# Kernel tuning notes

Measured on AMD Instinct MI355X. Metric: run time of the kernel, lower is better.

Reference implementation:

```python
import jax, jax.numpy as jnp
import numpy as np

NUM_HEADS = 8
EPS = 1e-5


def setup_inputs() -> dict:
    key = jax.random.key(0)
    ks = jax.random.split(key, 7)
    B, C, H, W, D = 1, 256, 16, 16, 16
    return {
        "x": jax.random.normal(ks[0], (B, C, H, W, D), dtype=jnp.float32),
        "w_dw": jax.random.normal(ks[1], (C, 1, 3, 3, 3), dtype=jnp.float32) * 0.05,
        "b_dw": jax.random.normal(ks[2], (C,), dtype=jnp.float32) * 0.05,
        "w_qkv": jax.random.normal(ks[3], (3 * C, C), dtype=jnp.float32) * 0.05,
        "b_qkv": jax.random.normal(ks[4], (3 * C,), dtype=jnp.float32) * 0.05,
        "w_proj": jax.random.normal(ks[5], (C, C), dtype=jnp.float32) * 0.05,
        "b_proj": jax.random.normal(ks[6], (C,), dtype=jnp.float32) * 0.05,
    }


def reference(x, w_dw, b_dw, w_qkv, b_qkv, w_proj, b_proj):
    B, C, H, W, D = x.shape
    nh = NUM_HEADS
    hd = C // nh
    scale = hd ** (-0.5)
    N = H * W * D

    # depthwise 3x3x3 conv (groups=C), SAME padding
    y = jax.lax.conv_general_dilated(
        x, w_dw, window_strides=(1, 1, 1), padding="SAME",
        dimension_numbers=("NCHWD", "OIHWD", "NCHWD"),
        feature_group_count=C,
    ) + b_dw[None, :, None, None, None]

    # InstanceNorm3d (affine=False): normalize over spatial dims per (b, c)
    mu = y.mean(axis=(2, 3, 4), keepdims=True)
    var = y.var(axis=(2, 3, 4), keepdims=True)
    y = (y - mu) * jax.lax.rsqrt(var + EPS)

    # 1x1x1 conv -> 3*C channels
    qkv = jnp.einsum("bchwd,oc->bohwd", y, w_qkv) + b_qkv[None, :, None, None, None]

    # [B, 3, nh, hd, N] -> q, k, v each [B, nh, N, hd]
    qkv = qkv.reshape(B, 3, nh, hd, N)
    q, k, v = jnp.transpose(qkv, (1, 0, 2, 4, 3))

    attn = jax.nn.softmax(jnp.einsum("bhnd,bhmd->bhnm", q, k) * scale, axis=-1)
    out = jnp.einsum("bhnm,bhmd->bhnd", attn, v)  # [B, nh, N, hd]

    # transpose(-1, -2) then reshape to [B, C, H, W, D]
    out = jnp.transpose(out, (0, 1, 3, 2)).reshape(B, C, H, W, D)

    # output 1x1x1 projection
    out = jnp.einsum("bchwd,oc->bohwd", out, w_proj) + b_proj[None, :, None, None, None]
    return out
```

## Files before the change

kernel.cpp:

```cpp
#include <hip/hip_runtime.h>
#include <hip/hip_bf16.h>

#define NSP 4096
#define QSC2 0.25503486f

typedef __attribute__((ext_vector_type(8))) short bf16x8;
typedef __attribute__((ext_vector_type(4))) float f32x4;
typedef __attribute__((ext_vector_type(16))) float f32x16;

__device__ __forceinline__ unsigned short f2bf(float f){
  union{float f;unsigned int u;}c; c.f=f;
  unsigned int r = c.u + 0x7fffu + ((c.u>>16)&1u);
  return (unsigned short)(r>>16);
}
__device__ __forceinline__ unsigned int pk2(float a, float b){
  __hip_bfloat162 p = __float22bfloat162_rn(make_float2(a, b));
  unsigned int r; __builtin_memcpy(&r, &p, 4); return r;
}
__device__ __forceinline__ ushort4 pk4(float a, float b, float c, float d){
  union { ushort4 u4; uint2 u2; } u;
  u.u2.x = pk2(a, b); u.u2.y = pk2(c, d);
  return u.u4;
}
__device__ __forceinline__ float bfu2f(unsigned short u){
  union { unsigned int i; float f; } c; c.i = ((unsigned int)u) << 16; return c.f;
}

__global__ __launch_bounds__(512) void k_dwconv(
    const float* __restrict__ x,
    const float* __restrict__ wdw,
    unsigned short* __restrict__ ybn)
{
  const int c = blockIdx.x;
  const int tid = threadIdx.x;
  __shared__ float xs[4096];
  __shared__ float wsh[27];
  __shared__ float rs[8], rq[8];

  const float* xc = x + (size_t)c * NSP;
  {
    const float4 a = ((const float4*)xc)[tid*2];
    const float4 b = ((const float4*)xc)[tid*2 + 1];
    *(float4*)&xs[tid*8]     = a;
    *(float4*)&xs[tid*8 + 4] = b;
  }
  if (tid < 27) wsh[tid] = wdw[c*27 + tid];
  __syncthreads();

  const int h = tid >> 5, w = (tid >> 1) & 15, d0 = (tid & 1) * 8;
  float acc[8] = {};
  #pragma unroll
  for (int kh = 0; kh < 3; kh++){
    const int hh = h + kh - 1;
    if ((unsigned)hh >= 16u) continue;
    #pragma unroll
    for (int kw = 0; kw < 3; kw++){
      const int ww = w + kw - 1;
      if ((unsigned)ww >= 16u) continue;
      const float* rowp = &xs[((hh << 4) + ww) << 4];
      float win[10];
      const float4 c0 = *(const float4*)&rowp[d0];
      const float4 c1 = *(const float4*)&rowp[d0 + 4];
      win[1] = c0.x; win[2] = c0.y; win[3] = c0.z; win[4] = c0.w;
      win[5] = c1.x; win[6] = c1.y; win[7] = c1.z; win[8] = c1.w;
      const float e7 = rowp[7], e8 = rowp[8];
      win[0] = d0 ? e7 : 0.f;
      win[9] = d0 ? 0.f : e8;
      #pragma unroll
      for (int kd = 0; kd < 3; kd++){
        const float wv = wsh[kh*9 + kw*3 + kd];
        #pragma unroll
        for (int j = 0; j < 8; j++) acc[j] += wv * win[j + kd];
      }
    }
  }

  float sum = 0.f, sumsq = 0.f;
  #pragma unroll
  for (int j = 0; j < 8; j++){ sum += acc[j]; sumsq += acc[j]*acc[j]; }
  #pragma unroll
  for (int off = 32; off > 0; off >>= 1){
    sum   += __shfl_down(sum, off, 64);
    sumsq += __shfl_down(sumsq, off, 64);
  }
  const int wid = tid >> 6, lane = tid & 63;
  if (lane == 0){ rs[wid] = sum; rq[wid] = sumsq; }
  __syncthreads();
  float ts = 0.f, tq = 0.f;
  #pragma unroll
  for (int i = 0; i < 8; i++){ ts += rs[i]; tq += rq[i]; }
  const float mean = ts * (1.f/4096.f);
  const float var  = tq * (1.f/4096.f) - mean*mean;
  const float rinv = rsqrtf(var + 1e-5f);

  unsigned short* yo = ybn + (size_t)c * NSP + tid*8;
  *(ushort4*)yo =
      pk4((acc[0]-mean)*rinv, (acc[1]-mean)*rinv, (acc[2]-mean)*rinv, (acc[3]-mean)*rinv);
  *(ushort4*)(yo + 4) =
      pk4((acc[4]-mean)*rinv, (acc[5]-mean)*rinv, (acc[6]-mean)*rinv, (acc[7]-mean)*rinv);
}

__global__ __launch_bounds__(256) void k_trans(
    const unsigned short* __restrict__ ybn,
    unsigned short* __restrict__ ynT)
{
  __shared__ unsigned short T[64][72];
  const int tid = threadIdx.x;
  const int n0 = blockIdx.x * 64, c0 = blockIdx.y * 64;
  const int cl = tid >> 4, n4 = (tid & 15) * 4;
  #pragma unroll
  for (int i = 0; i < 4; i++){
    const int c = cl + i*16;
    const ushort4 v = *(const ushort4*)(ybn + (size_t)(c0 + c) * NSP + n0 + n4);
    T[n4+0][c] = v.x; T[n4+1][c] = v.y; T[n4+2][c] = v.z; T[n4+3][c] = v.w;
  }
  __syncthreads();
  const int nl = tid >> 2, s8 = (tid & 3) * 16;
  *(uint4*)(ynT + (size_t)(n0+nl)*256 + c0 + s8)     = *(const uint4*)&T[nl][s8];
  *(uint4*)(ynT + (size_t)(n0+nl)*256 + c0 + s8 + 8) = *(const uint4*)&T[nl][s8 + 8];
}

__global__ __launch_bounds__(256) void k_qkv(
    const float* __restrict__ wqkv,
    const float* __restrict__ bqkv,
    const unsigned short* __restrict__ ynT,
    unsigned short* __restrict__ qb, unsigned short* __restrict__ kb,
    unsigned short* __restrict__ vbt)
{
  __shared__ unsigned short Wb[64][264];
  __shared__ float bsh[64];
  const int tid = threadIdx.x;
  const int o0 = blockIdx.y * 64;
  const int n0 = blockIdx.x * 64;
  {
    const int row = tid & 63, part = tid >> 6;
    const float* src = wqkv + (size_t)(o0 + row) * 256 + part * 64;
    unsigned short* dst = &Wb[row][part*64];
    #pragma unroll
    for (int j = 0; j < 8; j++){
      const float4 a = ((const float4*)src)[2*j];
      const float4 b = ((const float4*)src)[2*j+1];
      *(ushort4*)&dst[j*8]     = pk4(a.x, a.y, a.z, a.w);
      *(ushort4*)&dst[j*8 + 4] = pk4(b.x, b.y, b.z, b.w);
    }
    if (tid < 64) bsh[tid] = bqkv[o0 + tid];
  }
  __syncthreads();

  const int w = tid >> 6, lane = tid & 63, quad = lane >> 4, cc = lane & 15;
  const int nbase = n0 + w*16;
  const bool isv = (o0 >= 512);
  f32x4 acc[4] = {};

  #pragma unroll
  for (int k = 0; k < 8; k++){
    const bf16x8 y0 = *(const bf16x8*)(ynT + (size_t)(nbase + cc) * 256 + k*32 + quad*8);
    #pragma unroll
    for (int os = 0; os < 4; os++){
      const bf16x8 wf = *(const bf16x8*)&Wb[os*16 + cc][k*32 + quad*8];
      if (!isv) acc[os] = __builtin_amdgcn_mfma_f32_16x16x32_bf16(wf, y0, acc[os], 0, 0, 0);
      else      acc[os] = __builtin_amdgcn_mfma_f32_16x16x32_bf16(y0, wf, acc[os], 0, 0, 0);
    }
  }

  if (!isv){
    #pragma unroll
    for (int os = 0; os < 4; os++){
      const int obase = o0 + os*16 + quad*4;
      const int g = obase >> 8, hh = (obase >> 5) & 7, dd0 = obase & 31;
      const int n = nbase + cc;
      unsigned short* dst = (g == 0) ? qb : kb;
      const float sc = (g == 0) ? QSC2 : 1.f;
      const int bb = os*16 + quad*4;
      *(ushort4*)&dst[((size_t)hh * NSP + n) * 32 + dd0] =
          pk4((acc[os][0] + bsh[bb+0]) * sc, (acc[os][1] + bsh[bb+1]) * sc,
              (acc[os][2] + bsh[bb+2]) * sc, (acc[os][3] + bsh[bb+3]) * sc);
    }
  } else {
    #pragma unroll
    for (int os = 0; os < 4; os++){
      const int orow = o0 - 512 + os*16 + cc;
      const float bias = bsh[os*16 + cc];
      const int n4 = nbase + quad*4;
      *(ushort4*)&vbt[(size_t)orow * NSP + n4] =
          pk4(acc[os][0] + bias, acc[os][1] + bias, acc[os][2] + bias, acc[os][3] + bias);
    }
  }
}

__global__ __launch_bounds__(256) void k_attn(
    const unsigned short* __restrict__ qb,
    const unsigned short* __restrict__ kb,
    const unsigned short* __restrict__ vbt,
    unsigned short* __restrict__ opb, float* __restrict__ lp, int ktlen)
{
  const int h = blockIdx.y, q0 = blockIdx.x * 128, z = blockIdx.z;
  const int tid = threadIdx.x;
  const int w = tid >> 6, l = tid & 63;
  const int lq = l & 31, lb = l >> 5;

  __shared__ unsigned short ks [64][40];
  __shared__ unsigned short vsT[32][72];
  __shared__ unsigned short pst[128][72];

  const int qg = q0 + w*32 + lq;
  const bf16x8 qf0 = *(const bf16x8*)(qb + ((size_t)(h*NSP + qg))*32 + lb*8);
  const bf16x8 qf1 = *(const bf16x8*)(qb + ((size_t)(h*NSP + qg))*32 + 16 + lb*8);
  const unsigned short* kbase = kb  + (size_t)h * NSP * 32;
  const unsigned short* vbase = vbt + (size_t)h * 32 * NSP;

  f32x16 oacc = {};
  float lsum = 0.f;

  const int kt0 = z * ktlen;
  const int krow = tid >> 2, kseg = (tid & 3) * 8;
  const int vrow = tid >> 3, vseg = (tid & 7) * 8;
  const int iters = ktlen >> 6;

  for (int it = 0; it < iters; it++){
    const int kt = kt0 + it * 64;
    {
      *(uint4*)&ks[krow][kseg]  = *(const uint4*)(kbase + (size_t)(kt + krow) * 32 + kseg);
      *(uint4*)&vsT[vrow][vseg] = *(const uint4*)(vbase + (size_t)vrow * NSP + kt + vseg);
    }
    __syncthreads();

    #pragma unroll
    for (int t2 = 0; t2 < 2; t2++){
      const bf16x8 af0 = *(const bf16x8*)&ks[t2*32 + lq][lb*8];
      const bf16x8 af1 = *(const bf16x8*)&ks[t2*32 + lq][16 + lb*8];
      f32x16 sa = {};
      sa = __builtin_amdgcn_mfma_f32_32x32x16_bf16(af0, qf0, sa, 0, 0, 0);
      sa = __builtin_amdgcn_mfma_f32_32x32x16_bf16(af1, qf1, sa, 0, 0, 0);
      #pragma unroll
      for (int g = 0; g < 4; g++){
        const float p0 = __builtin_amdgcn_exp2f(sa[g*4+0]);
        const float p1 = __builtin_amdgcn_exp2f(sa[g*4+1]);
        const float p2 = __builtin_amdgcn_exp2f(sa[g*4+2]);
        const float p3 = __builtin_amdgcn_exp2f(sa[g*4+3]);
        lsum += (p0 + p1) + (p2 + p3);
        *(ushort4*)&pst[w*32 + lq][t2*32 + g*8 + lb*4] = pk4(p0, p1, p2, p3);
      }
    }
    #pragma unroll
    for (int ck = 0; ck < 4; ck++){
      const bf16x8 vf = *(const bf16x8*)&vsT[lq]       [ck*16 + lb*8];
      const bf16x8 pf = *(const bf16x8*)&pst[w*32 + lq][ck*16 + lb*8];
      oacc = __builtin_amdgcn_mfma_f32_32x32x16_bf16(vf, pf, oacc, 0, 0, 0);
    }
    __syncthreads();
  }

  lsum += __shfl_xor(lsum, 32, 64);

  unsigned short* dst = opb + ((size_t)z * NSP + qg) * 256 + h*32;
  #pragma unroll
  for (int g = 0; g < 4; g++){
    *(ushort4*)(dst + g*8 + lb*4) =
        pk4(oacc[g*4+0], oacc[g*4+1], oacc[g*4+2], oacc[g*4+3]);
  }
  if (lb == 0) lp[((size_t)z * 8 + h) * NSP + qg] = lsum;
}

__global__ __launch_bounds__(256) void k_proj(
    const float* __restrict__ wproj,
    const float* __restrict__ bproj,
    const unsigned short* __restrict__ opb,
    const float* __restrict__ lp,
    float* __restrict__ out, int nz)
{
  __shared__ unsigned short Wb[64][264];
  const int tid = threadIdx.x;
  const int o0 = blockIdx.y * 64;
  const int n0 = blockIdx.x * 64;
  {
    const int row = tid & 63, part = tid >> 6;
    const float* src = wproj + (size_t)(o0 + row) * 256 + part * 64;
    unsigned short* dst = &Wb[row][part*64];
    #pragma unroll
    for (int j = 0; j < 8; j++){
      const float4 a = ((const float4*)src)[2*j];
      const float4 b = ((const float4*)src)[2*j+1];
      *(ushort4*)&dst[j*8]     = pk4(a.x, a.y, a.z, a.w);
      *(ushort4*)&dst[j*8 + 4] = pk4(b.x, b.y, b.z, b.w);
    }
  }
  __syncthreads();

  const int w = tid >> 6, lane = tid & 63, quad = lane >> 4, cc = lane & 15;
  const int nbase = n0 + w*16;
  const int nr = nbase + cc;
  f32x4 acc[4] = {};

  #pragma unroll
  for (int k = 0; k < 8; k++){
    float lt = 0.f;
    float s[8] = {};
    for (int z = 0; z < nz; z++){
      lt += lp[((size_t)z*8 + k) * NSP + nr];
      union { uint4 q; unsigned short u[8]; } v;
      v.q = *(const uint4*)(opb + ((size_t)z * NSP + nr) * 256 + k*32 + quad*8);
      #pragma unroll
      for (int j = 0; j < 8; j++) s[j] += bfu2f(v.u[j]);
    }
    const float r = 1.f / lt;
    union { bf16x8 v; ushort4 u[2]; } yb;
    yb.u[0] = pk4(s[0]*r, s[1]*r, s[2]*r, s[3]*r);
    yb.u[1] = pk4(s[4]*r, s[5]*r, s[6]*r, s[7]*r);
    #pragma unroll
    for (int os = 0; os < 4; os++){
      const bf16x8 wf = *(const bf16x8*)&Wb[os*16 + cc][k*32 + quad*8];
      acc[os] = __builtin_amdgcn_mfma_f32_16x16x32_bf16(yb.v, wf, acc[os], 0, 0, 0);
    }
  }

  #pragma unroll
  for (int os = 0; os < 4; os++){
    const int o = o0 + os*16 + cc;
    const float bias = bproj[o];
    const int n4 = nbase + quad*4;
    *(float4*)&out[(size_t)o * NSP + n4] =
        make_float4(acc[os][0] + bias, acc[os][1] + bias,
                    acc[os][2] + bias, acc[os][3] + bias);
  }
}

extern "C" void kernel_launch(void* const* d_in, const int* in_sizes, int n_in,
                              void* d_out, int out_size, void* d_ws, size_t ws_size,
                              hipStream_t stream) {
  (void)in_sizes; (void)n_in; (void)out_size;
  const float* x     = (const float*)d_in[0];
  const float* wdw   = (const float*)d_in[1];
  const float* bdw   = (const float*)d_in[2];  (void)bdw;
  const float* wqkv  = (const float*)d_in[3];
  const float* bqkv  = (const float*)d_in[4];
  const float* wproj = (const float*)d_in[5];
  const float* bproj = (const float*)d_in[6];
  float* out = (float*)d_out;

  const int nz = (ws_size >= ((size_t)16 << 20)) ? 4 : 2;
  const int ktlen = NSP / nz;

  char* ws = (char*)d_ws;
  const size_t opB = (size_t)nz << 21;
  unsigned short* opb = (unsigned short*)ws;
  unsigned short* ybn = (unsigned short*)ws;
  unsigned short* ynT = (unsigned short*)(ws + (2<<20));
  unsigned short* qb  = (unsigned short*)(ws + opB);
  unsigned short* kb  = (unsigned short*)(ws + opB + (2<<20));
  unsigned short* vbt = (unsigned short*)(ws + opB + (4<<20));
  float*          lp  = (float*)(ws + opB + (6<<20));

  k_dwconv <<<dim3(256),        dim3(512), 0, stream>>>(x, wdw, ybn);
  k_trans  <<<dim3(64, 4),      dim3(256), 0, stream>>>(ybn, ynT);
  k_qkv    <<<dim3(64, 12),     dim3(256), 0, stream>>>(wqkv, bqkv, ynT, qb, kb, vbt);
  k_attn   <<<dim3(32, 8, nz),  dim3(256), 0, stream>>>(qb, kb, vbt, opb, lp, ktlen);
  k_proj   <<<dim3(64, 4),      dim3(256), 0, stream>>>(wproj, bproj, opb, lp, out, nz);
}
```

Baseline: 145.5 us.

## Fuse transpose into QKV kernel, widen dwconv blocks, split proj output tiles

Removes the separate transpose kernel. The QKV GEMM now loads its 64-token by 256-channel activation tile from the channel-major buffer and transposes it in shared memory, which saves one launch and a 2 MB round trip through global memory. The depthwise conv now runs 1024 threads per channel, each computing 4 outputs, and the projection kernel uses 32-row output tiles to double its grid. The costs are extra shared memory and redundant transposed loads in the QKV kernel (each tile is reloaded by 12 output blocks), strided 8-byte global reads, and bank conflicts on the scalar shared stores.

```diff
diff --git a/kernel.cpp b/kernel.cpp
--- a/kernel.cpp
+++ b/kernel.cpp
@@ -26,7 +26,7 @@
   union { unsigned int i; float f; } c; c.i = ((unsigned int)u) << 16; return c.f;
 }
 
-__global__ __launch_bounds__(512) void k_dwconv(
+__global__ __launch_bounds__(1024) void k_dwconv(
     const float* __restrict__ x,
     const float* __restrict__ wdw,
     unsigned short* __restrict__ ybn)
@@ -35,20 +35,15 @@
   const int tid = threadIdx.x;
   __shared__ float xs[4096];
   __shared__ float wsh[27];
-  __shared__ float rs[8], rq[8];
+  __shared__ float rs[16], rq[16];
 
   const float* xc = x + (size_t)c * NSP;
-  {
-    const float4 a = ((const float4*)xc)[tid*2];
-    const float4 b = ((const float4*)xc)[tid*2 + 1];
-    *(float4*)&xs[tid*8]     = a;
-    *(float4*)&xs[tid*8 + 4] = b;
-  }
+  *(float4*)&xs[tid*4] = ((const float4*)xc)[tid];
   if (tid < 27) wsh[tid] = wdw[c*27 + tid];
   __syncthreads();
 
-  const int h = tid >> 5, w = (tid >> 1) & 15, d0 = (tid & 1) * 8;
-  float acc[8] = {};
+  const int h = tid >> 6, w = (tid >> 2) & 15, d0 = (tid & 3) * 4;
+  float acc[4] = {};
   #pragma unroll
   for (int kh = 0; kh < 3; kh++){
     const int hh = h + kh - 1;
@@ -58,26 +53,23 @@
       const int ww = w + kw - 1;
       if ((unsigned)ww >= 16u) continue;
       const float* rowp = &xs[((hh << 4) + ww) << 4];
-      float win[10];
+      float win[6];
       const float4 c0 = *(const float4*)&rowp[d0];
-      const float4 c1 = *(const float4*)&rowp[d0 + 4];
       win[1] = c0.x; win[2] = c0.y; win[3] = c0.z; win[4] = c0.w;
-      win[5] = c1.x; win[6] = c1.y; win[7] = c1.z; win[8] = c1.w;
-      const float e7 = rowp[7], e8 = rowp[8];
-      win[0] = d0 ? e7 : 0.f;
-      win[9] = d0 ? 0.f : e8;
+      win[0] = d0        ? rowp[d0 - 1] : 0.f;
+      win[5] = (d0 < 12) ? rowp[d0 + 4] : 0.f;
       #pragma unroll
       for (int kd = 0; kd < 3; kd++){
         const float wv = wsh[kh*9 + kw*3 + kd];
         #pragma unroll
-        for (int j = 0; j < 8; j++) acc[j] += wv * win[j + kd];
+        for (int j = 0; j < 4; j++) acc[j] += wv * win[j + kd];
       }
     }
   }
 
   float sum = 0.f, sumsq = 0.f;
   #pragma unroll
-  for (int j = 0; j < 8; j++){ sum += acc[j]; sumsq += acc[j]*acc[j]; }
+  for (int j = 0; j < 4; j++){ sum += acc[j]; sumsq += acc[j]*acc[j]; }
   #pragma unroll
   for (int off = 32; off > 0; off >>= 1){
     sum   += __shfl_down(sum, off, 64);
@@ -88,46 +80,24 @@
   __syncthreads();
   float ts = 0.f, tq = 0.f;
   #pragma unroll
-  for (int i = 0; i < 8; i++){ ts += rs[i]; tq += rq[i]; }
+  for (int i = 0; i < 16; i++){ ts += rs[i]; tq += rq[i]; }
   const float mean = ts * (1.f/4096.f);
   const float var  = tq * (1.f/4096.f) - mean*mean;
   const float rinv = rsqrtf(var + 1e-5f);
 
-  unsigned short* yo = ybn + (size_t)c * NSP + tid*8;
-  *(ushort4*)yo =
+  *(ushort4*)(ybn + (size_t)c * NSP + tid*4) =
       pk4((acc[0]-mean)*rinv, (acc[1]-mean)*rinv, (acc[2]-mean)*rinv, (acc[3]-mean)*rinv);
-  *(ushort4*)(yo + 4) =
-      pk4((acc[4]-mean)*rinv, (acc[5]-mean)*rinv, (acc[6]-mean)*rinv, (acc[7]-mean)*rinv);
-}
-
-__global__ __launch_bounds__(256) void k_trans(
-    const unsigned short* __restrict__ ybn,
-    unsigned short* __restrict__ ynT)
-{
-  __shared__ unsigned short T[64][72];
-  const int tid = threadIdx.x;
-  const int n0 = blockIdx.x * 64, c0 = blockIdx.y * 64;
-  const int cl = tid >> 4, n4 = (tid & 15) * 4;
-  #pragma unroll
-  for (int i = 0; i < 4; i++){
-    const int c = cl + i*16;
-    const ushort4 v = *(const ushort4*)(ybn + (size_t)(c0 + c) * NSP + n0 + n4);
-    T[n4+0][c] = v.x; T[n4+1][c] = v.y; T[n4+2][c] = v.z; T[n4+3][c] = v.w;
-  }
-  __syncthreads();
-  const int nl = tid >> 2, s8 = (tid & 3) * 16;
-  *(uint4*)(ynT + (size_t)(n0+nl)*256 + c0 + s8)     = *(const uint4*)&T[nl][s8];
-  *(uint4*)(ynT + (size_t)(n0+nl)*256 + c0 + s8 + 8) = *(const uint4*)&T[nl][s8 + 8];
 }
 
 __global__ __launch_bounds__(256) void k_qkv(
     const float* __restrict__ wqkv,
     const float* __restrict__ bqkv,
-    const unsigned short* __restrict__ ynT,
+    const unsigned short* __restrict__ ybn,
     unsigned short* __restrict__ qb, unsigned short* __restrict__ kb,
     unsigned short* __restrict__ vbt)
 {
   __shared__ unsigned short Wb[64][264];
+  __shared__ unsigned short Ys[64][264];
   __shared__ float bsh[64];
   const int tid = threadIdx.x;
   const int o0 = blockIdx.y * 64;
@@ -145,6 +115,15 @@
     }
     if (tid < 64) bsh[tid] = bqkv[o0 + tid];
   }
+  {
+    const int cl = tid >> 4, n4 = (tid & 15) * 4;
+    #pragma unroll
+    for (int i = 0; i < 16; i++){
+      const int c = cl * 16 + i;
+      const ushort4 v = *(const ushort4*)(ybn + (size_t)c * NSP + n0 + n4);
+      Ys[n4+0][c] = v.x; Ys[n4+1][c] = v.y; Ys[n4+2][c] = v.z; Ys[n4+3][c] = v.w;
+    }
+  }
   __syncthreads();
 
   const int w = tid >> 6, lane = tid & 63, quad = lane >> 4, cc = lane & 15;
@@ -154,7 +133,7 @@
 
   #pragma unroll
   for (int k = 0; k < 8; k++){
-    const bf16x8 y0 = *(const bf16x8*)(ynT + (size_t)(nbase + cc) * 256 + k*32 + quad*8);
+    const bf16x8 y0 = *(const bf16x8*)&Ys[w*16 + cc][k*32 + quad*8];
     #pragma unroll
     for (int os = 0; os < 4; os++){
       const bf16x8 wf = *(const bf16x8*)&Wb[os*16 + cc][k*32 + quad*8];
@@ -269,16 +248,16 @@
     const float* __restrict__ lp,
     float* __restrict__ out, int nz)
 {
-  __shared__ unsigned short Wb[64][264];
+  __shared__ unsigned short Wb[32][264];
   const int tid = threadIdx.x;
-  const int o0 = blockIdx.y * 64;
+  const int o0 = blockIdx.y * 32;
   const int n0 = blockIdx.x * 64;
   {
-    const int row = tid & 63, part = tid >> 6;
-    const float* src = wproj + (size_t)(o0 + row) * 256 + part * 64;
-    unsigned short* dst = &Wb[row][part*64];
-    #pragma unroll
-    for (int j = 0; j < 8; j++){
+    const int row = tid & 31, part = tid >> 5;
+    const float* src = wproj + (size_t)(o0 + row) * 256 + part * 32;
+    unsigned short* dst = &Wb[row][part*32];
+    #pragma unroll
+    for (int j = 0; j < 4; j++){
       const float4 a = ((const float4*)src)[2*j];
       const float4 b = ((const float4*)src)[2*j+1];
       *(ushort4*)&dst[j*8]     = pk4(a.x, a.y, a.z, a.w);
@@ -290,7 +269,7 @@
   const int w = tid >> 6, lane = tid & 63, quad = lane >> 4, cc = lane & 15;
   const int nbase = n0 + w*16;
   const int nr = nbase + cc;
-  f32x4 acc[4] = {};
+  f32x4 acc[2] = {};
 
   #pragma unroll
   for (int k = 0; k < 8; k++){
@@ -308,14 +287,14 @@
     yb.u[0] = pk4(s[0]*r, s[1]*r, s[2]*r, s[3]*r);
     yb.u[1] = pk4(s[4]*r, s[5]*r, s[6]*r, s[7]*r);
     #pragma unroll
-    for (int os = 0; os < 4; os++){
+    for (int os = 0; os < 2; os++){
       const bf16x8 wf = *(const bf16x8*)&Wb[os*16 + cc][k*32 + quad*8];
       acc[os] = __builtin_amdgcn_mfma_f32_16x16x32_bf16(yb.v, wf, acc[os], 0, 0, 0);
     }
   }
 
   #pragma unroll
-  for (int os = 0; os < 4; os++){
+  for (int os = 0; os < 2; os++){
     const int o = o0 + os*16 + cc;
     const float bias = bproj[o];
     const int n4 = nbase + quad*4;
@@ -345,15 +324,13 @@
   const size_t opB = (size_t)nz << 21;
   unsigned short* opb = (unsigned short*)ws;
   unsigned short* ybn = (unsigned short*)ws;
-  unsigned short* ynT = (unsigned short*)(ws + (2<<20));
   unsigned short* qb  = (unsigned short*)(ws + opB);
   unsigned short* kb  = (unsigned short*)(ws + opB + (2<<20));
   unsigned short* vbt = (unsigned short*)(ws + opB + (4<<20));
   float*          lp  = (float*)(ws + opB + (6<<20));
 
-  k_dwconv <<<dim3(256),        dim3(512), 0, stream>>>(x, wdw, ybn);
-  k_trans  <<<dim3(64, 4),      dim3(256), 0, stream>>>(ybn, ynT);
-  k_qkv    <<<dim3(64, 12),     dim3(256), 0, stream>>>(wqkv, bqkv, ynT, qb, kb, vbt);
-  k_attn   <<<dim3(32, 8, nz),  dim3(256), 0, stream>>>(qb, kb, vbt, opb, lp, ktlen);
-  k_proj   <<<dim3(64, 4),      dim3(256), 0, stream>>>(wproj, bproj, opb, lp, out, nz);
-}
+  k_dwconv <<<dim3(256),        dim3(1024), 0, stream>>>(x, wdw, ybn);
+  k_qkv    <<<dim3(64, 12),     dim3(256),  0, stream>>>(wqkv, bqkv, ybn, qb, kb, vbt);
+  k_attn   <<<dim3(32, 8, nz),  dim3(256),  0, stream>>>(qb, kb, vbt, opb, lp, ktlen);
+  k_proj   <<<dim3(64, 8),      dim3(256),  0, stream>>>(wproj, bproj, opb, lp, out, nz);
+}
```

Result: faster. 140.5 us (-3.4%).
